# Kernel tuning notes

Hardware: AMD Instinct MI355X
Metric: run time of the kernel (lower is better)

The kernel has to match this reference:

```python
import jax, jax.numpy as jnp
import numpy as np

MARGIN = 1.0
NUM_CLASSES = 64

def setup_inputs() -> dict:
    key = jax.random.key(0)
    k1, k2 = jax.random.split(key)
    embeddings = jax.random.normal(k1, (4096, 512), dtype=jnp.float32)
    labels = jax.random.randint(k2, (4096,), 0, NUM_CLASSES, dtype=jnp.int64)
    return {"embeddings": embeddings, "labels": labels}

def _pairwise_dist(x):
    # Euclidean cdist via GEMM: ||xi||^2 + ||xj||^2 - 2 xi.xj, with a
    # grad-safe sqrt (zero distance -> zero, no nan gradient).
    sq_norms = jnp.sum(x * x, axis=1)                      # [B]
    sq = sq_norms[:, None] + sq_norms[None, :] - 2.0 * (x @ x.T)
    sq = jnp.maximum(sq, 0.0)
    pos = sq > 0.0
    return jnp.where(pos, jnp.sqrt(jnp.where(pos, sq, 1.0)), 0.0)

def reference(embeddings, labels):
    B = embeddings.shape[0]
    # L2 normalize (normalize=True)
    emb = embeddings / jnp.maximum(
        jnp.linalg.norm(embeddings, axis=1, keepdims=True), 1e-12)
    dist = _pairwise_dist(emb)                             # [B, B]
    same = labels[:, None] == labels[None, :]              # [B, B]
    eye = jnp.eye(B, dtype=bool)
    pos_mask = same & ~eye
    neg_mask = ~same
    pos_cnt = jnp.sum(pos_mask, axis=1)                    # [B]
    neg_cnt = jnp.sum(neg_mask, axis=1)
    # hard_positive=False -> mean over positive distances
    pos_stat = jnp.sum(jnp.where(pos_mask, dist, 0.0), axis=1) / jnp.maximum(pos_cnt, 1)
    # hardest negative = masked min (infinity trick)
    neg_stat = jnp.min(jnp.where(neg_mask, dist, jnp.inf), axis=1)
    per_row = jnp.maximum(pos_stat - neg_stat + MARGIN, 0.0)
    valid = (pos_cnt > 0) & (neg_cnt > 0)
    n_valid = jnp.sum(valid)
    total = jnp.sum(jnp.where(valid, per_row, 0.0))
    # reduction='mean' over valid rows; 0.0 if none valid
    return jnp.where(n_valid > 0, total / jnp.maximum(n_valid, 1), 0.0)
```

## Files before the change

### kernel.cpp

```cpp
#include <hip/hip_runtime.h>
#include <hip/hip_bf16.h>

#define BSZ 4096
#define DIM 512
#define NCLS 64
#define MARGIN_F 1.0f
#define NT 32
#define NBLK (NT * NT)
#define NSL (2 * NT)
#define NFIN 16

typedef short short8 __attribute__((ext_vector_type(8)));
typedef float floatx4 __attribute__((ext_vector_type(4)));
typedef unsigned short u16;

#define OFF_PP  (BSZ * DIM * 2)
#define OFF_PN  (OFF_PP + NSL * BSZ * 4)
#define OFF_ACC (OFF_PN + NSL * BSZ * 4)

__device__ __forceinline__ u16 f2bf_rne(float f) {
    unsigned x = __float_as_uint(f);
    x += 0x7FFFu + ((x >> 16) & 1u);
    return (u16)(x >> 16);
}

__device__ __forceinline__ void gld_lds16(const u16* g, u16* l) {
    __builtin_amdgcn_global_load_lds(
        (const __attribute__((address_space(1))) unsigned int*)g,
        (__attribute__((address_space(3))) unsigned int*)l, 16, 0, 0);
}

__global__ __launch_bounds__(256) void ht_normalize(
        const float* __restrict__ emb, u16* __restrict__ ebf,
        float* __restrict__ acc_total, int* __restrict__ acc_nv,
        int* __restrict__ counter2) {
    const int lane = threadIdx.x & 63;
    const int row = blockIdx.x * 4 + (threadIdx.x >> 6);
    const float4* r4 = (const float4*)(emb + (size_t)row * DIM);
    float4 v0 = r4[lane * 2];
    float4 v1 = r4[lane * 2 + 1];
    float s = v0.x * v0.x + v0.y * v0.y + v0.z * v0.z + v0.w * v0.w
            + v1.x * v1.x + v1.y * v1.y + v1.z * v1.z + v1.w * v1.w;
#pragma unroll
    for (int off = 1; off < 64; off <<= 1) s += __shfl_xor(s, off);
    const float inv = 1.0f / fmaxf(sqrtf(s), 1e-12f);

    uint4 o;
    o.x = (unsigned)f2bf_rne(v0.x * inv) | ((unsigned)f2bf_rne(v0.y * inv) << 16);
    o.y = (unsigned)f2bf_rne(v0.z * inv) | ((unsigned)f2bf_rne(v0.w * inv) << 16);
    o.z = (unsigned)f2bf_rne(v1.x * inv) | ((unsigned)f2bf_rne(v1.y * inv) << 16);
    o.w = (unsigned)f2bf_rne(v1.z * inv) | ((unsigned)f2bf_rne(v1.w * inv) << 16);
    ((uint4*)(ebf + (size_t)row * DIM))[lane] = o;

    if (blockIdx.x == 0 && threadIdx.x == 0) {
        *acc_total = 0.0f; *acc_nv = 0; *counter2 = 0;
    }
}

__global__ __launch_bounds__(256) void ht_gemm_reduce(
        const u16* __restrict__ ebf, const int* __restrict__ labels,
        float* __restrict__ part_ps, unsigned* __restrict__ part_nm) {
    __shared__ u16 sA[2][128 * 32];
    __shared__ u16 sB[2][128 * 32];
    __shared__ int sLI[128];
    __shared__ int sLJ[128];

    const int t = threadIdx.x;
    const int by = blockIdx.x >> 5;
    const int bx = blockIdx.x & 31;
    const int row0 = by * 128;
    const int col0 = bx * 128;

    if (t < 128) sLI[t] = labels[row0 + t];
    else         sLJ[t - 128] = labels[col0 + t - 128];

    const int lane = t & 63;
    const int wave = t >> 6;
    const int wr = (wave >> 1) * 64;
    const int wc = (wave & 1) * 64;
    const int l15 = lane & 15;
    const int quad = lane >> 4;

    const int s0 = t, s1 = 256 + t;
    const int gr0 = (s0 & 3) ^ ((s0 >> 3) & 3);
    const int gr1 = (s1 & 3) ^ ((s1 >> 3) & 3);
    const u16* gA0 = ebf + (size_t)(row0 + (s0 >> 2)) * DIM + gr0 * 8;
    const u16* gA1 = ebf + (size_t)(row0 + (s1 >> 2)) * DIM + gr1 * 8;
    const u16* gB0 = ebf + (size_t)(col0 + (s0 >> 2)) * DIM + gr0 * 8;
    const u16* gB1 = ebf + (size_t)(col0 + (s1 >> 2)) * DIM + gr1 * 8;
    const int lb0 = wave * 64 * 8;
    const int lb1 = (256 + wave * 64) * 8;

    const int qsw = (quad ^ ((l15 >> 1) & 3)) * 8;

    floatx4 acc[4][4] = {};

    gld_lds16(gA0, &sA[0][lb0]);
    gld_lds16(gA1, &sA[0][lb1]);
    gld_lds16(gB0, &sB[0][lb0]);
    gld_lds16(gB1, &sB[0][lb1]);

    int cur = 0;
    for (int ks = 0; ks < DIM / 32; ++ks) {
        __syncthreads();
        if (ks + 1 < DIM / 32) {
            const int kb = (ks + 1) * 32;
            gld_lds16(gA0 + kb, &sA[cur ^ 1][lb0]);
            gld_lds16(gA1 + kb, &sA[cur ^ 1][lb1]);
            gld_lds16(gB0 + kb, &sB[cur ^ 1][lb0]);
            gld_lds16(gB1 + kb, &sB[cur ^ 1][lb1]);
        }
        short8 af[4], bf[4];
#pragma unroll
        for (int mi = 0; mi < 4; ++mi)
            af[mi] = *(const short8*)(&sA[cur][(wr + mi * 16 + l15) * 32 + qsw]);
#pragma unroll
        for (int ni = 0; ni < 4; ++ni)
            bf[ni] = *(const short8*)(&sB[cur][(wc + ni * 16 + l15) * 32 + qsw]);
#pragma unroll
        for (int mi = 0; mi < 4; ++mi)
#pragma unroll
            for (int ni = 0; ni < 4; ++ni)
                acc[mi][ni] = __builtin_amdgcn_mfma_f32_16x16x32_bf16(
                    af[mi], bf[ni], acc[mi][ni], 0, 0, 0);
        cur ^= 1;
    }

    const float INF = __uint_as_float(0x7F800000u);
    const int rslice = 2 * bx + (wc >> 6);
#pragma unroll
    for (int mi = 0; mi < 4; ++mi) {
        const int rbase = wr + mi * 16 + quad * 4;
#pragma unroll
        for (int r = 0; r < 4; ++r) {
            const int rloc = rbase + r;
            const int gi = row0 + rloc;
            const int rl = sLI[rloc];
            float ps = 0.0f, nm = INF;
#pragma unroll
            for (int ni = 0; ni < 4; ++ni) {
                const int cloc = wc + ni * 16 + l15;
                const int gj = col0 + cloc;
                const int cl = sLJ[cloc];
                const float d = __builtin_amdgcn_sqrtf(
                    fmaxf(2.0f - 2.0f * acc[mi][ni][r], 0.0f));
                if (rl == cl) { if (gi != gj) ps += d; }
                else          { nm = fminf(nm, d); }
            }
#pragma unroll
            for (int off = 1; off < 16; off <<= 1) {
                ps += __shfl_xor(ps, off);
                nm = fminf(nm, __shfl_xor(nm, off));
            }
            if (l15 == 0) {
                part_ps[rslice * BSZ + gi] = ps;
                part_nm[rslice * BSZ + gi] = __float_as_uint(nm);
            }
        }
    }
}

__global__ __launch_bounds__(256) void ht_finalize(
        const float* __restrict__ part_ps, const unsigned* __restrict__ part_nm,
        const int* __restrict__ labels, float* __restrict__ acc_total,
        int* __restrict__ acc_nv, int* __restrict__ counter2,
        float* __restrict__ out) {
    __shared__ int hist[NCLS];
    __shared__ float sT[4];
    __shared__ int sN[4];
    const int t = threadIdx.x;
    if (t < NCLS) hist[t] = 0;
    __syncthreads();
    for (int i = t; i < BSZ; i += 256) atomicAdd(&hist[labels[i]], 1);
    __syncthreads();

    const int j = blockIdx.x * 256 + t;
    float ps = 0.0f;
    float nm = __uint_as_float(0x7F800000u);
#pragma unroll 8
    for (int s = 0; s < NSL; ++s) {
        ps += part_ps[s * BSZ + j];
        nm = fminf(nm, __uint_as_float(part_nm[s * BSZ + j]));
    }
    const int cnt = hist[labels[j]];
    const int pc = cnt - 1;
    const int nc = BSZ - cnt;
    float loss = 0.0f;
    int lv = 0;
    if (pc > 0 && nc > 0) {
        loss = fmaxf(ps / (float)pc - nm + MARGIN_F, 0.0f);
        lv = 1;
    }
#pragma unroll
    for (int off = 1; off < 64; off <<= 1) {
        loss += __shfl_xor(loss, off);
        lv += __shfl_xor(lv, off);
    }
    if ((t & 63) == 0) { sT[t >> 6] = loss; sN[t >> 6] = lv; }
    __syncthreads();
    if (t == 0) {
        const float tt = sT[0] + sT[1] + sT[2] + sT[3];
        const int nn = sN[0] + sN[1] + sN[2] + sN[3];
        __hip_atomic_fetch_add(acc_total, tt, __ATOMIC_ACQ_REL,
                               __HIP_MEMORY_SCOPE_AGENT);
        __hip_atomic_fetch_add(acc_nv, nn, __ATOMIC_ACQ_REL,
                               __HIP_MEMORY_SCOPE_AGENT);
        const int old2 = __hip_atomic_fetch_add(counter2, 1, __ATOMIC_ACQ_REL,
                                                __HIP_MEMORY_SCOPE_AGENT);
        if (old2 == NFIN - 1) {
            const float ft = __hip_atomic_load(acc_total, __ATOMIC_ACQUIRE,
                                               __HIP_MEMORY_SCOPE_AGENT);
            const int fn = __hip_atomic_load(acc_nv, __ATOMIC_ACQUIRE,
                                             __HIP_MEMORY_SCOPE_AGENT);
            out[0] = (fn > 0) ? ft / (float)fn : 0.0f;
        }
    }
}

extern "C" void kernel_launch(void* const* d_in, const int* in_sizes, int n_in,
                              void* d_out, int out_size, void* d_ws, size_t ws_size,
                              hipStream_t stream) {
    const float* emb = (const float*)d_in[0];
    const int* labels = (const int*)d_in[1];
    float* out = (float*)d_out;
    char* ws = (char*)d_ws;

    u16* ebf = (u16*)ws;
    float* part_ps = (float*)(ws + OFF_PP);
    unsigned* part_nm = (unsigned*)(ws + OFF_PN);
    float* acc_total = (float*)(ws + OFF_ACC);
    int* acc_nv = (int*)(ws + OFF_ACC + 4);
    int* counter2 = (int*)(ws + OFF_ACC + 8);

    ht_normalize<<<BSZ / 4, 256, 0, stream>>>(emb, ebf, acc_total, acc_nv,
                                              counter2);
    ht_gemm_reduce<<<NBLK, 256, 0, stream>>>(ebf, labels, part_ps, part_nm);
    ht_finalize<<<NFIN, 256, 0, stream>>>(part_ps, part_nm, labels,
                                          acc_total, acc_nv, counter2, out);
}
```

Measured before the change: 105.3 us.

## Exploit symmetry of Gram matrix by computing only upper-triangular tiles

```diff
diff --git a/kernel.cpp b/kernel.cpp
--- a/kernel.cpp
+++ b/kernel.cpp
@@ -6,7 +6,7 @@
 #define NCLS 64
 #define MARGIN_F 1.0f
 #define NT 32
-#define NBLK (NT * NT)
+#define NPAIR (NT * (NT + 1) / 2)
 #define NSL (2 * NT)
 #define NFIN 16
 
@@ -65,9 +65,12 @@
     __shared__ int sLI[128];
     __shared__ int sLJ[128];
 
+    int rem = blockIdx.x, by = 0;
+    while (rem >= NT - by) { rem -= NT - by; ++by; }
+    const int bx = by + rem;
+    const bool offd = (bx != by);
+
     const int t = threadIdx.x;
-    const int by = blockIdx.x >> 5;
-    const int bx = blockIdx.x & 31;
     const int row0 = by * 128;
     const int col0 = bx * 128;
 
@@ -128,6 +131,8 @@
 
     const float INF = __uint_as_float(0x7F800000u);
     const int rslice = 2 * bx + (wc >> 6);
+    float psc[4] = {0.f, 0.f, 0.f, 0.f};
+    float nmc[4] = {INF, INF, INF, INF};
 #pragma unroll
     for (int mi = 0; mi < 4; ++mi) {
         const int rbase = wr + mi * 16 + quad * 4;
@@ -144,8 +149,13 @@
                 const int cl = sLJ[cloc];
                 const float d = __builtin_amdgcn_sqrtf(
                     fmaxf(2.0f - 2.0f * acc[mi][ni][r], 0.0f));
-                if (rl == cl) { if (gi != gj) ps += d; }
-                else          { nm = fminf(nm, d); }
+                if (rl == cl) {
+                    if (gi != gj) ps += d;
+                    if (offd) psc[ni] += d;
+                } else {
+                    nm = fminf(nm, d);
+                    if (offd) nmc[ni] = fminf(nmc[ni], d);
+                }
             }
 #pragma unroll
             for (int off = 1; off < 16; off <<= 1) {
@@ -155,6 +165,21 @@
             if (l15 == 0) {
                 part_ps[rslice * BSZ + gi] = ps;
                 part_nm[rslice * BSZ + gi] = __float_as_uint(nm);
+            }
+        }
+    }
+    if (offd) {
+        const int cslice = 2 * by + (wr >> 6);
+#pragma unroll
+        for (int ni = 0; ni < 4; ++ni) {
+            float ps = psc[ni], nm = nmc[ni];
+            ps += __shfl_xor(ps, 16); ps += __shfl_xor(ps, 32);
+            nm = fminf(nm, __shfl_xor(nm, 16));
+            nm = fminf(nm, __shfl_xor(nm, 32));
+            if (quad == 0) {
+                const int gj = col0 + wc + ni * 16 + l15;
+                part_ps[cslice * BSZ + gj] = ps;
+                part_nm[cslice * BSZ + gj] = __float_as_uint(nm);
             }
         }
     }
@@ -234,7 +259,7 @@
 
     ht_normalize<<<BSZ / 4, 256, 0, stream>>>(emb, ebf, acc_total, acc_nv,
                                               counter2);
-    ht_gemm_reduce<<<NBLK, 256, 0, stream>>>(ebf, labels, part_ps, part_nm);
+    ht_gemm_reduce<<<NPAIR, 256, 0, stream>>>(ebf, labels, part_ps, part_nm);
     ht_finalize<<<NFIN, 256, 0, stream>>>(part_ps, part_nm, labels,
                                           acc_total, acc_nv, counter2, out);
 }
```

Result: faster. 95.77 us (-9.0%).
